# Kernel tuning notes

Measured on AMD Instinct MI355X. Metric: run time of the kernel, lower is better.

Reference implementation:

```python
import jax, jax.numpy as jnp
import numpy as np

NG, SNG, NS, SNS, NR = 4, 2, 4, 2, 3
NW = 4
STEP = 1 + NG + SNG + NS + SNS + NR  # 16
T, D = 512, 64
MARGIN, ALPHA, BETA, P, R = 1.0, 0.01, 1.0, 0.1, 0.1
KNUM, KMUL = 5, 2.0
GAMMA = 5.0          # soft-dtw gamma
BIG = 1e9            # finite 'inf' so softmin grads stay NaN-free
SIZ = NW * (NW + 1) // 2  # mmds buffer size in the original (zero padded)


def setup_inputs() -> dict:
    key = jax.random.key(0)
    k1, k2 = jax.random.split(key)
    data = jax.random.normal(k1, (NW * STEP, T, D), dtype=jnp.float32)
    lens = jax.random.randint(k2, (NW * STEP,), 64, T + 1, dtype=jnp.int32)
    return {"data": data, "lens": lens}


def _softdtw(Dmat, la, lb):
    """Soft-DTW via anti-diagonal scan. Dmat: (T,T) squared-euclid costs.
    Returns R[la, lb]; DP cells only depend on smaller indices so padding is inert."""
    Tn = Dmat.shape[0]
    idx = jnp.arange(Tn)

    def step(carry, k):
        r2, r1 = carry                      # diagonals k-2 and k-1, indexed by i
        j = k - idx
        valid = (j >= 0) & (j < Tn)
        d = jnp.where(valid, Dmat[idx, jnp.clip(j, 0, Tn - 1)], BIG)
        up = jnp.where(idx > 0, jnp.roll(r1, 1), BIG)     # cell (i-1, j)
        left = r1                                          # cell (i, j-1)
        diag = jnp.where(idx > 0, jnp.roll(r2, 1), BIG)    # cell (i-1, j-1)
        diag = jnp.where((idx == 0) & (k == 0), 0.0, diag)  # R[0,0] = 0 border
        m = jnp.stack([diag, up, left])
        softmin = -GAMMA * jax.nn.logsumexp(-m / GAMMA, axis=0)
        r = jnp.where(valid, d + softmin, BIG)
        return (r1, r), r

    init = (jnp.full((Tn,), BIG, Dmat.dtype), jnp.full((Tn,), BIG, Dmat.dtype))
    _, rows = jax.lax.scan(step, init, jnp.arange(2 * Tn - 1))
    # rows[k, i] = R[i+1, k-i+1]; want R[la, lb] -> k = la+lb-2, i = la-1
    return rows[la + lb - 2, la - 1]


def _mmd(x, y):
    """Multi-kernel Gaussian MMD (DAN-style MMDLoss), n == m."""
    n = x.shape[0]
    total = jnp.concatenate([x, y], axis=0)          # (2n, F)
    sq = jnp.sum(total * total, axis=1)
    l2 = sq[:, None] + sq[None, :] - 2.0 * (total @ total.T)
    ns = total.shape[0]
    bw = jnp.sum(l2) / (ns * ns - ns)
    bw = bw / (KMUL ** (KNUM // 2))
    bws = bw * (KMUL ** jnp.arange(KNUM, dtype=total.dtype))
    kern = jnp.sum(jnp.exp(-l2[None] / bws[:, None, None]), axis=0)
    XX, YY, XY, YX = kern[:n, :n], kern[n:, n:], kern[:n, n:], kern[n:, :n]
    return jnp.mean(XX + YY - XY - YX)


def _forward(data, lens):
    d = data.reshape(NW, STEP, T, D)
    li = lens.reshape(NW, STEP)
    Lf = li.astype(data.dtype)
    anchors = d[:, 0]          # (nw, T, D)
    others = d[:, 1:]          # (nw, 15, T, D)

    # squared-euclidean cost matrices via GEMM: (nw, 15, T, T)
    a2 = jnp.sum(anchors * anchors, -1)                      # (nw, T)
    b2 = jnp.sum(others * others, -1)                        # (nw, 15, T)
    ab = jnp.einsum('wtd,wjsd->wjts', anchors, others)
    cost = a2[:, None, :, None] + b2[:, :, None, :] - 2.0 * ab

    laB = jnp.broadcast_to(li[:, :1], (NW, STEP - 1))
    sdt = jax.vmap(jax.vmap(_softdtw))(cost, laB, li[:, 1:])  # (nw, 15)
    dist = sdt / (Lf[:, :1] + Lf[:, 1:])

    dist_g = dist[:, :NG + SNG]    # genuine + synthetic genuine (6)
    dist_n = dist[:, NG + SNG:]    # skilled + syn skilled + random (9)

    lk = jax.nn.relu(dist_g[:, :, None] + MARGIN - dist_n[:, None, :])
    ca = jnp.mean(dist_g, axis=1)
    cb = jnp.mean(dist_n[:, :5], axis=1)
    intra = jnp.sum(dist_g - ca[:, None], axis=1)
    inter = jax.nn.relu(BETA - jnp.abs(ca - cb))
    nz = jnp.sum(lk != 0, axis=(1, 2))
    lv = jnp.sum(lk, axis=(1, 2)) / (nz + 1).astype(data.dtype)
    total_loss = jnp.mean(lv + intra * P + inter * R)

    # MMD over all (i, j) pairs written by the original loop (i in 0..nw-1,
    # j in 1..nw-1, i != j); buffer zero-padded to SIZ, then max * alpha.
    groups = d[:, :STEP - 5].reshape(NW, STEP - 5, T * D)
    pi = jnp.array([0, 0, 0, 1, 1, 2, 2, 3, 3])
    pj = jnp.array([1, 2, 3, 2, 3, 1, 3, 1, 2])
    mmds = jax.vmap(_mmd)(groups[pi], groups[pj])
    mmds = jnp.concatenate([mmds, jnp.zeros((SIZ - pi.shape[0],), data.dtype)])
    mmd1 = jnp.max(mmds) * ALPHA
    return total_loss + mmd1


def reference(data, lens):
    return _forward(data, lens)
```

## Files before the change

### kernel.cpp

```cpp
#include <hip/hip_runtime.h>
#include <hip/hip_bf16.h>

#define TT   512
#define DD   64
#define NWK  4
#define STP  16
#define NPJ  15
#define NBLK 60
#define CMAT (TT * TT)
#define CSCALE 0.2885390081777927f
#define USCALE 3.4657359027997265f
#define BIGC   2.885390081777927e8f

#define SA 132

__global__ __launch_bounds__(256) void cost_kernel(const float* __restrict__ data,
                                                   const int* __restrict__ lens,
                                                   float* __restrict__ cost, int base) {
  int blk = base + blockIdx.z;
  int w = blk / NPJ, j = blk - w * NPJ;
  int la = lens[w * STP];
  int lb = lens[w * STP + 1 + j];
  int ti = blockIdx.y, tj = blockIdx.x;
  if (ti * 128 >= la || tj * 128 >= lb) return;

  __shared__ float As[DD][SA];
  __shared__ float Bs[DD][SA];
  __shared__ float a2[128], b2[128];

  const float* A = data + ((size_t)(w * STP) * TT + (size_t)ti * 128) * DD;
  const float* B = data + ((size_t)(w * STP + 1 + j) * TT + (size_t)tj * 128) * DD;
  int t = threadIdx.x;

  #pragma unroll
  for (int i = 0; i < 8; ++i) {
    int idx = t + i * 256;
    int r = idx & 127;
    int kq = idx >> 7;
    float4 va = *(const float4*)(A + r * DD + kq * 4);
    As[kq * 4 + 0][r] = va.x; As[kq * 4 + 1][r] = va.y;
    As[kq * 4 + 2][r] = va.z; As[kq * 4 + 3][r] = va.w;
    float4 vb = *(const float4*)(B + r * DD + kq * 4);
    Bs[kq * 4 + 0][r] = vb.x; Bs[kq * 4 + 1][r] = vb.y;
    Bs[kq * 4 + 2][r] = vb.z; Bs[kq * 4 + 3][r] = vb.w;
  }
  __syncthreads();
  if (t < 128) {
    float s = 0.f;
    for (int k = 0; k < DD; ++k) { float x = As[k][t]; s += x * x; }
    a2[t] = s;
  } else {
    float s = 0.f;
    for (int k = 0; k < DD; ++k) { float x = Bs[k][t - 128]; s += x * x; }
    b2[t - 128] = s;
  }
  __syncthreads();

  int r0 = (t >> 4) << 2;
  int c0 = (t & 15) << 2;
  float acc[8][8];
  #pragma unroll
  for (int i = 0; i < 8; ++i)
    #pragma unroll
    for (int q = 0; q < 8; ++q) acc[i][q] = 0.f;

  #pragma unroll 2
  for (int k = 0; k < DD; ++k) {
    float4 aL = *(const float4*)&As[k][r0];
    float4 aH = *(const float4*)&As[k][r0 + 64];
    float4 bL = *(const float4*)&Bs[k][c0];
    float4 bH = *(const float4*)&Bs[k][c0 + 64];
    float a[8] = {aL.x, aL.y, aL.z, aL.w, aH.x, aH.y, aH.z, aH.w};
    float b[8] = {bL.x, bL.y, bL.z, bL.w, bH.x, bH.y, bH.z, bH.w};
    #pragma unroll
    for (int i = 0; i < 8; ++i)
      #pragma unroll
      for (int q = 0; q < 8; ++q)
        acc[i][q] += a[i] * b[q];
  }

  float* Cbase = cost + (size_t)blockIdx.z * CMAT;
  #pragma unroll
  for (int i = 0; i < 8; ++i) {
    int rr = (i < 4) ? (r0 + i) : (r0 + 60 + i);
    float ar = a2[rr];
    float* Crow = Cbase + (size_t)(ti * 128 + rr) * TT + tj * 128;
    float4 o;
    o.x = (ar + b2[c0 + 0] - 2.f * acc[i][0]) * CSCALE;
    o.y = (ar + b2[c0 + 1] - 2.f * acc[i][1]) * CSCALE;
    o.z = (ar + b2[c0 + 2] - 2.f * acc[i][2]) * CSCALE;
    o.w = (ar + b2[c0 + 3] - 2.f * acc[i][3]) * CSCALE;
    *(float4*)(Crow + c0) = o;
    float4 o2;
    o2.x = (ar + b2[c0 + 64] - 2.f * acc[i][4]) * CSCALE;
    o2.y = (ar + b2[c0 + 65] - 2.f * acc[i][5]) * CSCALE;
    o2.z = (ar + b2[c0 + 66] - 2.f * acc[i][6]) * CSCALE;
    o2.w = (ar + b2[c0 + 67] - 2.f * acc[i][7]) * CSCALE;
    *(float4*)(Crow + c0 + 64) = o2;
  }
}

__device__ __forceinline__ float dpcell(float dc, float a, float b, float c) {
  float mn = fminf(fminf(a, b), c);
  float mx = fmaxf(fmaxf(a, b), c);
  float md = __builtin_amdgcn_fmed3f(a, b, c);
  float e = 1.0f + __builtin_amdgcn_exp2f(mn - md) + __builtin_amdgcn_exp2f(mn - mx);
  return dc + mn - __builtin_amdgcn_logf(e);
}

__device__ __forceinline__ float wave_shr1(float x) {
  int xi = __float_as_int(x);
  int r = __builtin_amdgcn_update_dpp(xi, xi, 0x138 , 0xF, 0xF, false);
  return __int_as_float(r);
}

__global__ __launch_bounds__(256) void dp_gram_kernel(const float* __restrict__ cost,
                                                      const int* __restrict__ lens,
                                                      const float* __restrict__ data,
                                                      float* __restrict__ sdt,
                                                      float* __restrict__ gram,
                                                      int base, int ndp) {
  int bid = blockIdx.x;

  if (bid >= ndp) {
    __shared__ float red[4][16];
    int g = bid - ndp;
    int bx = g / 11, by = g - bx * 11;
    int t = threadIdx.x;
    const float* Ar[4]; const float* Br[4];
    #pragma unroll
    for (int a = 0; a < 4; ++a) {
      int gx = bx * 4 + a;
      Ar[a] = data + (size_t)((gx / 11) * STP + gx % 11) * (TT * DD);
      int gy = by * 4 + a;
      Br[a] = data + (size_t)((gy / 11) * STP + gy % 11) * (TT * DD);
    }
    float acc[4][4];
    #pragma unroll
    for (int a = 0; a < 4; ++a)
      #pragma unroll
      for (int b = 0; b < 4; ++b) acc[a][b] = 0.f;
    for (int k = t * 4; k < TT * DD; k += 1024) {
      float4 av[4], bv[4];
      #pragma unroll
      for (int a = 0; a < 4; ++a) av[a] = *(const float4*)(Ar[a] + k);
      #pragma unroll
      for (int b = 0; b < 4; ++b) bv[b] = *(const float4*)(Br[b] + k);
      #pragma unroll
      for (int a = 0; a < 4; ++a)
        #pragma unroll
        for (int b = 0; b < 4; ++b)
          acc[a][b] += av[a].x * bv[b].x + av[a].y * bv[b].y +
                       av[a].z * bv[b].z + av[a].w * bv[b].w;
    }
    int wave = t >> 6, lane = t & 63;
    #pragma unroll
    for (int a = 0; a < 4; ++a)
      #pragma unroll
      for (int b = 0; b < 4; ++b) {
        float v = acc[a][b];
        for (int off = 32; off > 0; off >>= 1) v += __shfl_down(v, off);
        if (lane == 0) red[wave][a * 4 + b] = v;
      }
    __syncthreads();
    if (t < 16) {
      float v = red[0][t] + red[1][t] + red[2][t] + red[3][t];
      int a = t >> 2, b = t & 3;
      gram[(size_t)(bx * 4 + a) * 44 + by * 4 + b] = v;
    }
    return;
  }

  __shared__ float bufB[3][600];
  __shared__ int flags[4];

  if (threadIdx.x < 4) flags[threadIdx.x] = 0;
  __syncthreads();

  int blk = base + bid;
  int w = blk / NPJ, j = blk - w * NPJ;
  int la = lens[w * STP];
  int lb = lens[w * STP + 1 + j];
  const float* C = cost + (size_t)bid * CMAT;

  int q = threadIdx.x >> 6, ln = threadIdx.x & 63;
  int c0 = q * 128 + ln * 2;
  const float* Cp = C + c0;

  int qt = (lb - 1) >> 7;
  int lt = ((lb - 1) >> 1) & 63;
  int par = (lb - 1) & 1;
  int rt = la - 1;
  bool isT = (q == qt) && (ln == lt);

  float U0 = BIGC, U1 = BIGC;
  float NL = BIGC;
  float NLd = (q == 0 && ln == 0) ? 0.0f : BIGC;
  float v1s = BIGC;
  float res = 0.0f;

  int ngrp = (la + 70) >> 3;

  float2 cc[8], cn[8];
  #pragma unroll
  for (int k = 0; k < 8; ++k) {
    int rr = k - ln; rr = rr < 0 ? 0 : (rr > 511 ? 511 : rr);
    cc[k] = *(const float2*)(Cp + (size_t)rr * TT);
  }
  float bb[8];

  for (int g = 0; g < ngrp; ++g) {
    if (q > 0) {
      int need = 8 * g + 9; if (need > la) need = la;
      while (*(volatile int*)&flags[q - 1] < need) __builtin_amdgcn_s_sleep(2);
      __threadfence_block();
      #pragma unroll
      for (int k = 0; k < 8; ++k) bb[k] = bufB[q - 1][8 * g + 1 + k];
      if (g == 0) {
        float nl0 = bufB[q - 1][0];
        if (ln == 0) NL = nl0;
      }
    }
    #pragma unroll
    for (int k = 0; k < 8; ++k) {
      int rr = 8 * (g + 1) + k - ln; rr = rr < 0 ? 0 : (rr > 511 ? 511 : rr);
      cn[k] = *(const float2*)(Cp + (size_t)rr * TT);
    }
    #pragma unroll
    for (int k = 0; k < 8; ++k) {
      int r = 8 * g + k - ln;
      bool act = ((unsigned)r < 512u);
      if (act) {
        float v0 = dpcell(cc[k].x, NLd, U0, NL);
        float v1 = dpcell(cc[k].y, U0, U1, v0);
        if (isT & (r == rt)) res = par ? v1 : v0;
        NLd = NL; U0 = v0; U1 = v1; v1s = v1;
        if (q < 3 && ln == 63) {
          bufB[q][r] = v1;
          if ((r & 7) == 7) {
            __threadfence_block();
            *(volatile int*)&flags[q] = r + 1;
          }
        }
      }
      float nb = wave_shr1(v1s);
      if (ln == 0) nb = (q == 0) ? BIGC : bb[k];
      NL = nb;
    }
    #pragma unroll
    for (int k = 0; k < 8; ++k) cc[k] = cn[k];
  }
  if (q < 3 && ln == 63) {
    __threadfence_block();
    *(volatile int*)&flags[q] = 512;
  }
  if (isT) sdt[blk] = res * USCALE;
}

__global__ __launch_bounds__(640) void final_kernel(const float* __restrict__ sdt,
                                                    const int* __restrict__ lens,
                                                    const float* __restrict__ gram,
                                                    float* __restrict__ out) {
  __shared__ float partial[16];
  int t = threadIdx.x, wave = t >> 6, lane = t & 63;
  if (wave < 9) {
    const int piA[9] = {0, 0, 0, 1, 1, 2, 2, 3, 3};
    const int pjA[9] = {1, 2, 3, 2, 3, 1, 3, 1, 2};
    int P = piA[wave], Q = pjA[wave];
    float s1 = 0.f;
    for (int c = lane; c < 484; c += 64) {
      int i = c / 22, jj = c - (c / 22) * 22;
      int gi = (i < 11) ? P * 11 + i : Q * 11 + (i - 11);
      int gj = (jj < 11) ? P * 11 + jj : Q * 11 + (jj - 11);
      s1 += gram[gi * 44 + gi] + gram[gj * 44 + gj] - 2.f * gram[gi * 44 + gj];
    }
    for (int off = 32; off > 0; off >>= 1) s1 += __shfl_down(s1, off);
    s1 = __shfl(s1, 0);
    float bw = s1 / 462.0f * 0.25f;
    float inv[5];
    float b = bw;
    #pragma unroll
    for (int qq = 0; qq < 5; ++qq) { inv[qq] = -1.0f / b; b *= 2.0f; }
    float s2 = 0.f;
    for (int c = lane; c < 484; c += 64) {
      int i = c / 22, jj = c - (c / 22) * 22;
      int gi = (i < 11) ? P * 11 + i : Q * 11 + (i - 11);
      int gj = (jj < 11) ? P * 11 + jj : Q * 11 + (jj - 11);
      float l2 = gram[gi * 44 + gi] + gram[gj * 44 + gj] - 2.f * gram[gi * 44 + gj];
      float kk = 0.f;
      #pragma unroll
      for (int qq = 0; qq < 5; ++qq) kk += __expf(l2 * inv[qq]);
      float sgn = ((i < 11) == (jj < 11)) ? 1.0f : -1.0f;
      s2 += sgn * kk;
    }
    for (int off = 32; off > 0; off >>= 1) s2 += __shfl_down(s2, off);
    if (lane == 0) partial[wave] = s2 / 121.0f;
  } else {
    float term = 0.f;
    if (wave == 9 && lane < 4) {
      int w = lane;
      float L0 = (float)lens[w * STP];
      float dist[15];
      for (int qq = 0; qq < 15; ++qq)
        dist[qq] = sdt[w * NPJ + qq] / (L0 + (float)lens[w * STP + 1 + qq]);
      float ca = 0.f, cb = 0.f;
      for (int a = 0; a < 6; ++a) ca += dist[a];
      ca *= (1.0f / 6.0f);
      for (int bq = 6; bq < 11; ++bq) cb += dist[bq];
      cb *= (1.0f / 5.0f);
      float lksum = 0.f; int nz = 0;
      for (int a = 0; a < 6; ++a)
        for (int bq = 6; bq < 15; ++bq) {
          float x = dist[a] + 1.0f - dist[bq];
          if (x > 0.f) { lksum += x; nz += 1; }
        }
      float intra = 0.f;
      for (int a = 0; a < 6; ++a) intra += dist[a] - ca;
      float inter = fmaxf(0.f, 1.0f - fabsf(ca - cb));
      term = lksum / (float)(nz + 1) + intra * 0.1f + inter * 0.1f;
    }
    if (wave == 9) {
      term += __shfl_down(term, 1);
      term += __shfl_down(term, 2);
      if (lane == 0) partial[9] = term * 0.25f;
    }
  }
  __syncthreads();
  if (t == 0) {
    float mx = 0.0f;
    for (int p = 0; p < 9; ++p) mx = fmaxf(mx, partial[p]);
    out[0] = partial[9] + 0.01f * mx;
  }
}

extern "C" void kernel_launch(void* const* d_in, const int* in_sizes, int n_in,
                              void* d_out, int out_size, void* d_ws, size_t ws_size,
                              hipStream_t stream) {
  const float* data = (const float*)d_in[0];
  const int* lens = (const int*)d_in[1];
  float* out = (float*)d_out;

  float* sdtb  = (float*)d_ws;
  float* gramb = sdtb + 64;
  float* costb = (float*)((char*)d_ws + 8192);

  size_t avail = (ws_size > 8192) ? (ws_size - 8192) : 0;
  int chunk = (int)(avail / ((size_t)CMAT * sizeof(float)));
  if (chunk < 1) chunk = 1;
  if (chunk > NBLK) chunk = NBLK;

  bool first = true;
  for (int base = 0; base < NBLK; base += chunk) {
    int n = NBLK - base;
    if (n > chunk) n = chunk;
    cost_kernel<<<dim3(4, 4, n), 256, 0, stream>>>(data, lens, costb, base);
    int extra = first ? 121 : 0;
    dp_gram_kernel<<<n + extra, 256, 0, stream>>>(costb, lens, data, sdtb, gramb, base, n);
    first = false;
  }
  final_kernel<<<1, 640, 0, stream>>>(sdtb, lens, gramb, out);
}
```

Baseline: 208.6 us.

## Map one DP column per lane using eight waves instead of two per lane

The soft-DTW wavefront now uses 512 threads (8 waves of 64 lanes), each lane owning a single column rather than two, with inter-wave boundary handoff extended to 7 buffers and flags. This halves the serial dependent dpcell chain per lane step, shortening the critical path of the anti-diagonal DP. The cost is twice as many waves whose pipeline startup lags and handshakes add per-wave skew, plus scalar loads instead of float2. The gram branch is adapted to 512 threads and 8 reduction slots.

```diff
diff --git a/kernel.cpp b/kernel.cpp
--- a/kernel.cpp
+++ b/kernel.cpp
@@ -114,7 +114,7 @@
   return __int_as_float(r);
 }
 
-__global__ __launch_bounds__(256) void dp_gram_kernel(const float* __restrict__ cost,
+__global__ __launch_bounds__(512) void dp_gram_kernel(const float* __restrict__ cost,
                                                       const int* __restrict__ lens,
                                                       const float* __restrict__ data,
                                                       float* __restrict__ sdt,
@@ -123,7 +123,7 @@
   int bid = blockIdx.x;
 
   if (bid >= ndp) {
-    __shared__ float red[4][16];
+    __shared__ float red[8][16];
     int g = bid - ndp;
     int bx = g / 11, by = g - bx * 11;
     int t = threadIdx.x;
@@ -140,7 +140,7 @@
     for (int a = 0; a < 4; ++a)
       #pragma unroll
       for (int b = 0; b < 4; ++b) acc[a][b] = 0.f;
-    for (int k = t * 4; k < TT * DD; k += 1024) {
+    for (int k = t * 4; k < TT * DD; k += 2048) {
       float4 av[4], bv[4];
       #pragma unroll
       for (int a = 0; a < 4; ++a) av[a] = *(const float4*)(Ar[a] + k);
@@ -164,17 +164,19 @@
       }
     __syncthreads();
     if (t < 16) {
-      float v = red[0][t] + red[1][t] + red[2][t] + red[3][t];
+      float v = 0.f;
+      #pragma unroll
+      for (int ww = 0; ww < 8; ++ww) v += red[ww][t];
       int a = t >> 2, b = t & 3;
       gram[(size_t)(bx * 4 + a) * 44 + by * 4 + b] = v;
     }
     return;
   }
 
-  __shared__ float bufB[3][600];
-  __shared__ int flags[4];
-
-  if (threadIdx.x < 4) flags[threadIdx.x] = 0;
+  __shared__ float bufB[7][600];
+  __shared__ int flags[8];
+
+  if (threadIdx.x < 8) flags[threadIdx.x] = 0;
   __syncthreads();
 
   int blk = base + bid;
@@ -184,30 +186,32 @@
   const float* C = cost + (size_t)bid * CMAT;
 
   int q = threadIdx.x >> 6, ln = threadIdx.x & 63;
-  int c0 = q * 128 + ln * 2;
+  int c0 = q * 64 + ln;
   const float* Cp = C + c0;
 
-  int qt = (lb - 1) >> 7;
-  int lt = ((lb - 1) >> 1) & 63;
-  int par = (lb - 1) & 1;
+  int qt = (lb - 1) >> 6;
+  int lt = (lb - 1) & 63;
   int rt = la - 1;
   bool isT = (q == qt) && (ln == lt);
 
-  float U0 = BIGC, U1 = BIGC;
+  float U = BIGC;
   float NL = BIGC;
   float NLd = (q == 0 && ln == 0) ? 0.0f : BIGC;
-  float v1s = BIGC;
   float res = 0.0f;
 
   int ngrp = (la + 70) >> 3;
 
-  float2 cc[8], cn[8];
+  float cc[8], cn[8];
   #pragma unroll
   for (int k = 0; k < 8; ++k) {
     int rr = k - ln; rr = rr < 0 ? 0 : (rr > 511 ? 511 : rr);
-    cc[k] = *(const float2*)(Cp + (size_t)rr * TT);
+    cc[k] = Cp[(size_t)rr * TT];
   }
   float bb[8];
+  if (q == 0) {
+    #pragma unroll
+    for (int k = 0; k < 8; ++k) bb[k] = BIGC;
+  }
 
   for (int g = 0; g < ngrp; ++g) {
     if (q > 0) {
@@ -216,43 +220,39 @@
       __threadfence_block();
       #pragma unroll
       for (int k = 0; k < 8; ++k) bb[k] = bufB[q - 1][8 * g + 1 + k];
-      if (g == 0) {
-        float nl0 = bufB[q - 1][0];
-        if (ln == 0) NL = nl0;
-      }
+      if (g == 0 && ln == 0) NL = bufB[q - 1][0];
     }
     #pragma unroll
     for (int k = 0; k < 8; ++k) {
       int rr = 8 * (g + 1) + k - ln; rr = rr < 0 ? 0 : (rr > 511 ? 511 : rr);
-      cn[k] = *(const float2*)(Cp + (size_t)rr * TT);
+      cn[k] = Cp[(size_t)rr * TT];
     }
     #pragma unroll
     for (int k = 0; k < 8; ++k) {
       int r = 8 * g + k - ln;
       bool act = ((unsigned)r < 512u);
       if (act) {
-        float v0 = dpcell(cc[k].x, NLd, U0, NL);
-        float v1 = dpcell(cc[k].y, U0, U1, v0);
-        if (isT & (r == rt)) res = par ? v1 : v0;
-        NLd = NL; U0 = v0; U1 = v1; v1s = v1;
-        if (q < 3 && ln == 63) {
-          bufB[q][r] = v1;
-          if ((r & 7) == 7) {
+        float v = dpcell(cc[k], NLd, U, NL);
+        if (isT & (r == rt)) res = v;
+        NLd = NL; U = v;
+        if (q < 7 && ln == 63) {
+          bufB[q][r] = v;
+          if ((r & 7) == 0 || r == 511) {
             __threadfence_block();
             *(volatile int*)&flags[q] = r + 1;
           }
         }
       }
-      float nb = wave_shr1(v1s);
-      if (ln == 0) nb = (q == 0) ? BIGC : bb[k];
+      float nb = wave_shr1(U);
+      if (ln == 0) nb = bb[k];
       NL = nb;
     }
     #pragma unroll
     for (int k = 0; k < 8; ++k) cc[k] = cn[k];
   }
-  if (q < 3 && ln == 63) {
+  if (q < 7 && ln == 63) {
     __threadfence_block();
-    *(volatile int*)&flags[q] = 512;
+    *(volatile int*)&flags[q] = 600;
   }
   if (isT) sdt[blk] = res * USCALE;
 }
@@ -355,7 +355,7 @@
     if (n > chunk) n = chunk;
     cost_kernel<<<dim3(4, 4, n), 256, 0, stream>>>(data, lens, costb, base);
     int extra = first ? 121 : 0;
-    dp_gram_kernel<<<n + extra, 256, 0, stream>>>(costb, lens, data, sdtb, gramb, base, n);
+    dp_gram_kernel<<<n + extra, 512, 0, stream>>>(costb, lens, data, sdtb, gramb, base, n);
     first = false;
   }
   final_kernel<<<1, 640, 0, stream>>>(sdtb, lens, gramb, out);
```

After: 264.6 us. +26.9%, slower.
